# Kernel optimization log

Measured on AMD Instinct MI355X. Metric: run time of the kernel, lower is better.

The kernel has to match this reference:

```python
import jax, jax.numpy as jnp
import numpy as np

K = 8               # top-k frequencies
PRED_LEN = 96       # prediction_length
LOW_FREQ = 1        # low_frequency cutoff (drops DC)


def setup_inputs() -> dict:
    key = jax.random.key(0)
    x = jax.random.normal(key, (32, 2048, 64), dtype=jnp.float32)
    return {"x": x}


def reference(x):
    b, t, d = x.shape
    x_freq = jnp.fft.rfft(x, axis=1)                 # (b, t//2+1, d) complex
    freqs = jnp.fft.rfftfreq(t).astype(x.dtype)
    if t % 2 == 0:
        x_freq = x_freq[:, LOW_FREQ:-1]              # drop DC and Nyquist
        f = freqs[LOW_FREQ:-1]
    else:
        x_freq = x_freq[:, LOW_FREQ:]
        f = freqs[LOW_FREQ:]

    # top-k over frequency dim (axis=1), independently per (b, d)
    mag = jnp.abs(x_freq)                            # (b, F, d)
    _, idx = jax.lax.top_k(jnp.moveaxis(mag, 1, 2), K)  # (b, d, K), sorted desc
    idx = jnp.moveaxis(idx, 1, 2)                    # (b, K, d)
    x_k = jnp.take_along_axis(x_freq, idx, axis=1)   # (b, K, d) complex
    f_k = f[idx]                                     # (b, K, d)

    # extrapolate: add conjugate (negative) frequencies, then cos-sum
    x2 = jnp.concatenate([x_k, jnp.conj(x_k)], axis=1)  # (b, 2K, d)
    f2 = jnp.concatenate([f_k, -f_k], axis=1)           # (b, 2K, d)
    t_val = jnp.arange(t + PRED_LEN, dtype=x.dtype)     # (T,)
    amp = jnp.abs(x2) / t                               # (b, 2K, d)
    phase = jnp.angle(x2)                               # (b, 2K, d)
    # (b, 2K, T, d) broadcast intermediate, reduced over freq axis
    x_time = amp[:, :, None, :] * jnp.cos(
        2.0 * np.float32(np.pi) * f2[:, :, None, :] * t_val[None, None, :, None]
        + phase[:, :, None, :]
    )
    return x_time.sum(axis=1)                        # (b, t+PRED_LEN, d)
```

## Files before the change

kernel.cpp:

```cpp
#include <hip/hip_runtime.h>
#include <math.h>

#define BB 32
#define TT 2048
#define DD 64
#define PRED 96
#define TP (TT + PRED)
#define KTOP 8
#define MARGIN 8e-4f
#define PI_D 3.14159265358979323846

__device__ __forceinline__ int br6(int l) { return (int)(__brev((unsigned)l) >> 26); }
static constexpr int BR4[16] = {0,8,4,12,2,10,6,14,1,9,5,13,3,11,7,15};
static constexpr float C32T[16] = {
    1.0f, 0.98078528040323044913f, 0.92387953251128675613f, 0.83146961230254523708f,
    0.70710678118654752440f, 0.55557023301960222474f, 0.38268343236508977173f, 0.19509032201612826785f,
    0.0f, -0.19509032201612826785f, -0.38268343236508977173f, -0.55557023301960222474f,
    -0.70710678118654752440f, -0.83146961230254523708f, -0.92387953251128675613f, -0.98078528040323044913f};
static constexpr float S32T[16] = {
    0.0f, 0.19509032201612826785f, 0.38268343236508977173f, 0.55557023301960222474f,
    0.70710678118654752440f, 0.83146961230254523708f, 0.92387953251128675613f, 0.98078528040323044913f,
    1.0f, 0.98078528040323044913f, 0.92387953251128675613f, 0.83146961230254523708f,
    0.70710678118654752440f, 0.55557023301960222474f, 0.38268343236508977173f, 0.19509032201612826785f};

__device__ __forceinline__ float2 ctw(float2 a, int m) {
    const float rev = (float)m * (1.0f / 2048.0f);
    const float c = __builtin_amdgcn_cosf(rev);
    const float s = __builtin_amdgcn_sinf(rev);
    return make_float2(a.x * c + a.y * s, a.y * c - a.x * s);
}

#define SRE(pr,a) POOL[9216 + (pr) * 4224 + (a)]
#define SIM(pr,a) POOL[9216 + (pr) * 4224 + 2112 + (a)]

__global__ __launch_bounds__(256, 2) void fused_kernel(const float* __restrict__ x,
                                                       float* __restrict__ out) {
    __shared__ float POOL[17664];
    __shared__ int   coefK[4][KTOP];
    __shared__ float coefR[4][KTOP], coefI[4][KTOP];

    const int t    = threadIdx.x;
    const int wv   = t >> 6, p = t & 63;
    const int pair = wv >> 1, w = wv & 1;
    const int bid  = blockIdx.x;
    const int xcd  = bid & 7;
    const int idx  = bid >> 3;
    const int b    = (idx >> 3) * 4 + (xcd >> 1);
    const int grp4 = (xcd & 1) * 8 + (idx & 7);
    const int dp   = grp4 * 2 + pair;
    const int ch   = grp4 * 4 + wv;

    const float2* xv = (const float2*)x;
    const size_t xbase = (size_t)b * TT * (DD / 2) + dp;
    const int rl = 2 * br6(p) + w;

    float2 v[16];
    #pragma unroll
    for (int i = 0; i < 16; ++i)
        v[i] = xv[xbase + (size_t)(128 * BR4[i] + rl) * (DD / 2)];

    #pragma unroll
    for (int s = 1; s <= 4; ++s) {
        const int m = 1 << s, half = m >> 1, stepw = 32 >> s;
        #pragma unroll
        for (int g = 0; g < 16; g += m) {
            #pragma unroll
            for (int j = 0; j < half; ++j) {
                const float c = C32T[j * stepw], sn = S32T[j * stepw];
                const int i0 = g + j, i1 = i0 + half;
                const float tr = c * v[i1].x + sn * v[i1].y;
                const float ti = c * v[i1].y - sn * v[i1].x;
                v[i1] = make_float2(v[i0].x - tr, v[i0].y - ti);
                v[i0] = make_float2(v[i0].x + tr, v[i0].y + ti);
            }
        }
    }

    #pragma unroll
    for (int q = 1; q < 16; ++q) v[q] = ctw(v[q], (rl * q) & (TT - 1));

    #pragma unroll
    for (int s = 1; s <= 6; ++s) {
        const int half = 1 << (s - 1);
        const float rev = (float)(p & (half - 1)) / (float)(1 << s);
        const float wc  = __builtin_amdgcn_cosf(rev);
        const float wsn = __builtin_amdgcn_sinf(rev);
        const bool  hi  = (p & half) != 0;
        #pragma unroll
        for (int q = 0; q < 16; ++q) {
            float2 pv;
            pv.x = __shfl_xor(v[q].x, half, 64);
            pv.y = __shfl_xor(v[q].y, half, 64);
            const float2 bsv = hi ? v[q] : pv;
            const float2 asv = hi ? pv : v[q];
            const float tr = wc * bsv.x + wsn * bsv.y;
            const float ti = wc * bsv.y - wsn * bsv.x;
            v[q] = hi ? make_float2(asv.x - tr, asv.y - ti)
                      : make_float2(asv.x + tr, asv.y + ti);
        }
    }

    {
        const int exw = pair * 4608 + w * 2304 + p * 36;
        #pragma unroll
        for (int c = 0; c < 8; ++c)
            *(float4*)&POOL[exw + 4 * c] =
                make_float4(v[2*c].x, v[2*c].y, v[2*c+1].x, v[2*c+1].y);
    }
    __syncthreads();
    {
        const int exr = pair * 4608 + (1 - w) * 2304 + p * 36;
        const float revp = (float)p * (1.0f / 128.0f);
        const float wc7 = __builtin_amdgcn_cosf(revp);
        const float ws7 = __builtin_amdgcn_sinf(revp);
        const int kb = 1024 * w + 16 * p;
        #pragma unroll
        for (int c = 0; c < 8; ++c) {
            const float4 g = *(const float4*)&POOL[exr + 4 * c];
            #pragma unroll
            for (int e = 0; e < 2; ++e) {
                const int q = 2 * c + e;
                const float2 pv = e ? make_float2(g.z, g.w) : make_float2(g.x, g.y);
                const float2 bsv = w ? v[q] : pv;
                const float2 asv = w ? pv : v[q];
                const float tr = wc7 * bsv.x + ws7 * bsv.y;
                const float ti = wc7 * bsv.y - ws7 * bsv.x;
                const int k = kb + q, a = k + (k >> 5);
                SRE(pair, a) = w ? (asv.x - tr) : (asv.x + tr);
                SIM(pair, a) = w ? (asv.y - ti) : (asv.y + ti);
            }
        }
    }
    __syncthreads();

    unsigned A[16];
    #pragma unroll
    for (int q = 0; q < 16; ++q) {
        const int k = 16 * p + q;
        unsigned kk = 0u;
        if (k != 0) {
            const int a1 = k + (k >> 5);
            const int pk = TT - k, a2 = pk + (pk >> 5);
            const float zr = SRE(pair, a1), zi = SIM(pair, a1);
            const float yr = SRE(pair, a2), yi = SIM(pair, a2);
            float cr, ci;
            if (w == 0) { cr = 0.5f * (zr + yr); ci = 0.5f * (zi - yi); }
            else        { cr = 0.5f * (zi + yi); ci = 0.5f * (yr - zr); }
            const float mg = cr * cr + ci * ci;
            kk = (__float_as_uint(mg) & 0xFFFFF800u) | (unsigned)(2047 - k);
        }
        A[q] = kk;
    }

    #pragma unroll
    for (int sz = 2; sz <= 16; sz <<= 1) {
        #pragma unroll
        for (int d = sz >> 1; d > 0; d >>= 1) {
            #pragma unroll
            for (int i2 = 0; i2 < 16; ++i2) {
                const int j2i = i2 ^ d;
                if (j2i > i2) {
                    const bool desc = ((i2 & sz) == 0);
                    const unsigned a = A[i2], b2 = A[j2i];
                    const unsigned mx = a > b2 ? a : b2, mn = a > b2 ? b2 : a;
                    A[i2] = desc ? mx : mn;  A[j2i] = desc ? mn : mx;
                }
            }
        }
    }
    #pragma unroll
    for (int off = 1; off <= 32; off <<= 1) {
        unsigned Bv[16];
        #pragma unroll
        for (int i2 = 0; i2 < 16; ++i2)
            Bv[i2] = (unsigned)__shfl_xor((int)A[i2], off, 64);
        #pragma unroll
        for (int i2 = 0; i2 < 16; ++i2) {
            const unsigned o = Bv[15 - i2];
            A[i2] = A[i2] > o ? A[i2] : o;
        }
        #pragma unroll
        for (int d = 8; d > 0; d >>= 1) {
            #pragma unroll
            for (int i2 = 0; i2 < 16; ++i2) {
                if ((i2 & d) == 0) {
                    const int j2i = i2 + d;
                    const unsigned a = A[i2], b2 = A[j2i];
                    A[i2] = a > b2 ? a : b2;  A[j2i] = a > b2 ? b2 : a;
                }
            }
        }
    }

    const float m8f = __uint_as_float(A[7] & 0xFFFFF800u);
    unsigned bandmask = 0u;
    #pragma unroll
    for (int r = 0; r < 16; ++r) {
        const float mr = __uint_as_float(A[r] & 0xFFFFF800u);
        if (fabsf(mr - m8f) <= MARGIN * m8f) bandmask |= (1u << r);
    }
    const int flg = (bandmask != (1u << 7)) ? 1 : 0;

    unsigned myk = 0u;
    #pragma unroll
    for (int i2 = 0; i2 < 16; ++i2) myk = (p == i2) ? A[i2] : myk;
    const int kcand = 2047 - (int)(myk & 0x7FFu);

    if (!flg && p < KTOP) {
        const int k = kcand, a1 = k + (k >> 5), pk = TT - k, a2 = pk + (pk >> 5);
        const float zr = SRE(pair, a1), zi = SIM(pair, a1);
        const float yr = SRE(pair, a2), yi = SIM(pair, a2);
        float cr, ci;
        if (w == 0) { cr = 0.5f * (zr + yr); ci = 0.5f * (zi - yi); }
        else        { cr = 0.5f * (zi + yi); ci = 0.5f * (yr - zr); }
        coefK[wv][p] = k;
        coefR[wv][p] = cr * (2.0f / (float)TT);
        coefI[wv][p] = ci * (2.0f / (float)TT);
    }

    if (flg) {
        float sv[32];
        const float* xs = x + (size_t)b * TT * DD + ch;
        #pragma unroll
        for (int m2 = 0; m2 < 32; ++m2)
            sv[m2] = xs[(size_t)(p + 64 * m2) * DD];
        const double thA = -2.0 * PI_D * (double)p / 64.0;
        const double thB = -2.0 * PI_D * (double)p / (double)TT;
        const double wac = cos(thA), was = sin(thA);
        const double wbc = cos(thB), wbs = sin(thB);

        const unsigned bm = bandmask;
        const int lo = (int)__builtin_ctz(bm);
        double myM = 0.0, myR = 0.0, myI = 0.0;
        for (int r = 0; r < 16; ++r) {
            if (!((bm >> r) & 1u)) continue;
            const int kr = __shfl(kcand, r, 64);
            double ar = 0.0, ai = 0.0;
            for (int m2 = 0; m2 < 32; ++m2) {
                const int n  = p + 64 * m2;
                const int mm = (n * kr) & (TT - 1);
                const double qc  = __shfl(wac, mm >> 5, 64);
                const double qs  = __shfl(was, mm >> 5, 64);
                const double rc2 = __shfl(wbc, mm & 31, 64);
                const double rs2 = __shfl(wbs, mm & 31, 64);
                const double wr = qc * rc2 - qs * rs2;
                const double wi = qc * rs2 + qs * rc2;
                ar = fma((double)sv[m2], wr, ar);
                ai = fma((double)sv[m2], wi, ai);
            }
            #pragma unroll
            for (int off = 32; off; off >>= 1) {
                ar += __shfl_xor(ar, off, 64);
                ai += __shfl_xor(ai, off, 64);
            }
            if (p == r) { myM = ar * ar + ai * ai; myR = ar; myI = ai; }
        }
        const int h16 = p & 15;
        const double selfM = __shfl(myM, h16, 64);
        const int    selfK = __shfl(kcand, h16, 64);
        int rb = 0;
        for (int r2 = 0; r2 < 16; ++r2) {
            if (!((bm >> r2) & 1u)) continue;
            const double om = __shfl(myM, r2, 64);
            const int    ok = __shfl(kcand, r2, 64);
            if (r2 != h16 && (om > selfM || (om == selfM && ok < selfK))) ++rb;
        }
        const int isband = (int)((bm >> h16) & 1u);
        const int rank = isband ? (lo + rb) : h16;
        if (p < 16 && rank < KTOP) {
            coefK[wv][rank] = kcand;
            if (isband) {
                coefR[wv][rank] = (float)(myR * (2.0 / (double)TT));
                coefI[wv][rank] = (float)(myI * (2.0 / (double)TT));
            } else {
                const int k = kcand, a1 = k + (k >> 5), pk = TT - k, a2 = pk + (pk >> 5);
                const float zr = SRE(pair, a1), zi = SIM(pair, a1);
                const float yr = SRE(pair, a2), yi = SIM(pair, a2);
                float cr, ci;
                if (w == 0) { cr = 0.5f * (zr + yr); ci = 0.5f * (zi - yi); }
                else        { cr = 0.5f * (zi + yi); ci = 0.5f * (yr - zr); }
                coefR[wv][rank] = cr * (2.0f / (float)TT);
                coefI[wv][rank] = ci * (2.0f / (float)TT);
            }
        }
    }
    __syncthreads();

    const int d4 = t & 3, tq = t >> 2;
    int   kc[KTOP];
    float fr[KTOP], fi[KTOP], pc[KTOP], ps[KTOP], rc[KTOP], rs[KTOP];
    #pragma unroll
    for (int pp = 0; pp < KTOP; ++pp) {
        kc[pp] = coefK[d4][pp];
        fr[pp] = coefR[d4][pp];
        fi[pp] = coefI[d4][pp];
        const int j0 = (kc[pp] * tq) & (TT - 1);
        const float rv0 = (float)j0 * (1.0f / 2048.0f);
        pc[pp] = __builtin_amdgcn_cosf(rv0);
        ps[pp] = __builtin_amdgcn_sinf(rv0);
        const int jr = (kc[pp] * 64) & (TT - 1);
        const float rvr = (float)jr * (1.0f / 2048.0f);
        rc[pp] = __builtin_amdgcn_cosf(rvr);
        rs[pp] = __builtin_amdgcn_sinf(rvr);
    }
    float* ob = out + (size_t)b * TP * DD + grp4 * 4 + d4;
    #pragma unroll 2
    for (int m = 0; m < 34; ++m) {
        const int tv = tq + 64 * m;
        float acc = 0.0f;
        #pragma unroll
        for (int pp = 0; pp < KTOP; ++pp) acc += fr[pp] * pc[pp] - fi[pp] * ps[pp];
        if (tv < TP) ob[(size_t)tv * DD] = acc;
        #pragma unroll
        for (int pp = 0; pp < KTOP; ++pp) {
            const float nc = pc[pp] * rc[pp] - ps[pp] * rs[pp];
            const float ns = pc[pp] * rs[pp] + ps[pp] * rc[pp];
            pc[pp] = nc; ps[pp] = ns;
        }
    }
}

extern "C" void kernel_launch(void* const* d_in, const int* in_sizes, int n_in,
                              void* d_out, int out_size, void* d_ws, size_t ws_size,
                              hipStream_t stream) {
    const float* x = (const float*)d_in[0];
    float* out = (float*)d_out;
    (void)d_ws; (void)ws_size; (void)in_sizes; (void)n_in; (void)out_size;

    fused_kernel<<<BB * 16, 256, 0, stream>>>(x, out);
}
```

Before: 97.47 us.

## Split each channel pair's FFT across four waves to double the block count

Each block now handles one complex channel pair (two real channels) instead of two pairs. Each of the four waves holds 8 points instead of 16, and an extra cross-wave radix-2 stage is done through shared memory. Shared memory per block is roughly halved and launch bounds are raised to 4 blocks per CU, so the grid doubles to 1024 blocks for more occupancy and parallelism. In exchange there is an extra exchange round with its barriers, and only two of the four waves do the top-k selection, leaving the other waves idle during that phase.

```diff
diff --git a/kernel.cpp b/kernel.cpp
--- a/kernel.cpp
+++ b/kernel.cpp
@@ -11,7 +11,7 @@
 #define PI_D 3.14159265358979323846
 
 __device__ __forceinline__ int br6(int l) { return (int)(__brev((unsigned)l) >> 26); }
-static constexpr int BR4[16] = {0,8,4,12,2,10,6,14,1,9,5,13,3,11,7,15};
+static constexpr int BR3[8] = {0,4,2,6,1,5,3,7};
 static constexpr float C32T[16] = {
     1.0f, 0.98078528040323044913f, 0.92387953251128675613f, 0.83146961230254523708f,
     0.70710678118654752440f, 0.55557023301960222474f, 0.38268343236508977173f, 0.19509032201612826785f,
@@ -30,40 +30,39 @@
     return make_float2(a.x * c + a.y * s, a.y * c - a.x * s);
 }
 
-#define SRE(pr,a) POOL[9216 + (pr) * 4224 + (a)]
-#define SIM(pr,a) POOL[9216 + (pr) * 4224 + 2112 + (a)]
-
-__global__ __launch_bounds__(256, 2) void fused_kernel(const float* __restrict__ x,
+#define EXB(wvi,pi) ((wvi) * 1152 + (pi) * 18)
+#define SRE(a) POOL[4608 + (a)]
+#define SIM(a) POOL[6720 + (a)]
+
+__global__ __launch_bounds__(256, 4) void fused_kernel(const float* __restrict__ x,
                                                        float* __restrict__ out) {
-    __shared__ float POOL[17664];
-    __shared__ int   coefK[4][KTOP];
-    __shared__ float coefR[4][KTOP], coefI[4][KTOP];
+    __shared__ float POOL[8832];
+    __shared__ int   coefK[2][KTOP];
+    __shared__ float coefR[2][KTOP], coefI[2][KTOP];
 
     const int t    = threadIdx.x;
     const int wv   = t >> 6, p = t & 63;
-    const int pair = wv >> 1, w = wv & 1;
     const int bid  = blockIdx.x;
     const int xcd  = bid & 7;
     const int idx  = bid >> 3;
-    const int b    = (idx >> 3) * 4 + (xcd >> 1);
-    const int grp4 = (xcd & 1) * 8 + (idx & 7);
-    const int dp   = grp4 * 2 + pair;
-    const int ch   = grp4 * 4 + wv;
+    const int b    = ((idx >> 3) << 1) | (xcd >> 2);
+    const int dp   = ((xcd & 3) << 3) | (idx & 7);
 
     const float2* xv = (const float2*)x;
     const size_t xbase = (size_t)b * TT * (DD / 2) + dp;
-    const int rl = 2 * br6(p) + w;
-
-    float2 v[16];
-    #pragma unroll
-    for (int i = 0; i < 16; ++i)
-        v[i] = xv[xbase + (size_t)(128 * BR4[i] + rl) * (DD / 2)];
-
-    #pragma unroll
-    for (int s = 1; s <= 4; ++s) {
+    const int br2wv = ((wv & 1) << 1) | ((wv >> 1) & 1);
+    const int rl = 4 * br6(p) + br2wv;
+
+    float2 v[8];
+    #pragma unroll
+    for (int i = 0; i < 8; ++i)
+        v[i] = xv[xbase + (size_t)(256 * BR3[i] + rl) * (DD / 2)];
+
+    #pragma unroll
+    for (int s = 1; s <= 3; ++s) {
         const int m = 1 << s, half = m >> 1, stepw = 32 >> s;
         #pragma unroll
-        for (int g = 0; g < 16; g += m) {
+        for (int g = 0; g < 8; g += m) {
             #pragma unroll
             for (int j = 0; j < half; ++j) {
                 const float c = C32T[j * stepw], sn = S32T[j * stepw];
@@ -77,7 +76,7 @@
     }
 
     #pragma unroll
-    for (int q = 1; q < 16; ++q) v[q] = ctw(v[q], (rl * q) & (TT - 1));
+    for (int q = 1; q < 8; ++q) v[q] = ctw(v[q], (rl * q) & (TT - 1));
 
     #pragma unroll
     for (int s = 1; s <= 6; ++s) {
@@ -87,7 +86,7 @@
         const float wsn = __builtin_amdgcn_sinf(rev);
         const bool  hi  = (p & half) != 0;
         #pragma unroll
-        for (int q = 0; q < 16; ++q) {
+        for (int q = 0; q < 8; ++q) {
             float2 pv;
             pv.x = __shfl_xor(v[q].x, half, 64);
             pv.y = __shfl_xor(v[q].y, half, 64);
@@ -101,212 +100,236 @@
     }
 
     {
-        const int exw = pair * 4608 + w * 2304 + p * 36;
-        #pragma unroll
-        for (int c = 0; c < 8; ++c)
-            *(float4*)&POOL[exw + 4 * c] =
-                make_float4(v[2*c].x, v[2*c].y, v[2*c+1].x, v[2*c+1].y);
+        const int exw = EXB(wv, p);
+        #pragma unroll
+        for (int q = 0; q < 8; ++q) *(float2*)&POOL[exw + 2 * q] = v[q];
     }
     __syncthreads();
     {
-        const int exr = pair * 4608 + (1 - w) * 2304 + p * 36;
-        const float revp = (float)p * (1.0f / 128.0f);
-        const float wc7 = __builtin_amdgcn_cosf(revp);
-        const float ws7 = __builtin_amdgcn_sinf(revp);
-        const int kb = 1024 * w + 16 * p;
-        #pragma unroll
-        for (int c = 0; c < 8; ++c) {
-            const float4 g = *(const float4*)&POOL[exr + 4 * c];
-            #pragma unroll
-            for (int e = 0; e < 2; ++e) {
-                const int q = 2 * c + e;
-                const float2 pv = e ? make_float2(g.z, g.w) : make_float2(g.x, g.y);
-                const float2 bsv = w ? v[q] : pv;
-                const float2 asv = w ? pv : v[q];
-                const float tr = wc7 * bsv.x + ws7 * bsv.y;
-                const float ti = wc7 * bsv.y - ws7 * bsv.x;
-                const int k = kb + q, a = k + (k >> 5);
-                SRE(pair, a) = w ? (asv.x - tr) : (asv.x + tr);
-                SIM(pair, a) = w ? (asv.y - ti) : (asv.y + ti);
-            }
-        }
-    }
-    __syncthreads();
-
-    unsigned A[16];
-    #pragma unroll
-    for (int q = 0; q < 16; ++q) {
-        const int k = 16 * p + q;
-        unsigned kk = 0u;
-        if (k != 0) {
-            const int a1 = k + (k >> 5);
-            const int pk = TT - k, a2 = pk + (pk >> 5);
-            const float zr = SRE(pair, a1), zi = SIM(pair, a1);
-            const float yr = SRE(pair, a2), yi = SIM(pair, a2);
+        const int exr = EXB(wv ^ 1, p);
+        const float rev7 = (float)p * (1.0f / 128.0f);
+        const float c7 = __builtin_amdgcn_cosf(rev7);
+        const float s7 = __builtin_amdgcn_sinf(rev7);
+        const bool hi7 = (wv & 1) != 0;
+        #pragma unroll
+        for (int q = 0; q < 8; ++q) {
+            const float2 pv = *(const float2*)&POOL[exr + 2 * q];
+            const float2 bsv = hi7 ? v[q] : pv;
+            const float2 asv = hi7 ? pv : v[q];
+            const float tr = c7 * bsv.x + s7 * bsv.y;
+            const float ti = c7 * bsv.y - s7 * bsv.x;
+            v[q] = hi7 ? make_float2(asv.x - tr, asv.y - ti)
+                       : make_float2(asv.x + tr, asv.y + ti);
+        }
+    }
+    __syncthreads();
+
+    {
+        const int exw = EXB(wv, p);
+        #pragma unroll
+        for (int q = 0; q < 8; ++q) *(float2*)&POOL[exw + 2 * q] = v[q];
+    }
+    __syncthreads();
+    {
+        const int exr = EXB(wv ^ 2, p);
+        const float rev8 = (float)(64 * (wv & 1) + p) * (1.0f / 256.0f);
+        const float c8 = __builtin_amdgcn_cosf(rev8);
+        const float s8 = __builtin_amdgcn_sinf(rev8);
+        const bool hi8 = ((wv >> 1) & 1) != 0;
+        const int kb = 512 * wv + 8 * p;
+        #pragma unroll
+        for (int q = 0; q < 8; ++q) {
+            const float2 pv = *(const float2*)&POOL[exr + 2 * q];
+            const float2 bsv = hi8 ? v[q] : pv;
+            const float2 asv = hi8 ? pv : v[q];
+            const float tr = c8 * bsv.x + s8 * bsv.y;
+            const float ti = c8 * bsv.y - s8 * bsv.x;
+            const float re = hi8 ? (asv.x - tr) : (asv.x + tr);
+            const float im = hi8 ? (asv.y - ti) : (asv.y + ti);
+            const int k = kb + q, a = k + (k >> 5);
+            SRE(a) = re;
+            SIM(a) = im;
+        }
+    }
+    __syncthreads();
+
+    if (wv < 2) {
+        const int w = wv;
+        unsigned A[16];
+        #pragma unroll
+        for (int q = 0; q < 16; ++q) {
+            const int k = 16 * p + q;
+            unsigned kk = 0u;
+            if (k != 0) {
+                const int a1 = k + (k >> 5);
+                const int pk = TT - k, a2 = pk + (pk >> 5);
+                const float zr = SRE(a1), zi = SIM(a1);
+                const float yr = SRE(a2), yi = SIM(a2);
+                float cr, ci;
+                if (w == 0) { cr = 0.5f * (zr + yr); ci = 0.5f * (zi - yi); }
+                else        { cr = 0.5f * (zi + yi); ci = 0.5f * (yr - zr); }
+                const float mg = cr * cr + ci * ci;
+                kk = (__float_as_uint(mg) & 0xFFFFF800u) | (unsigned)(2047 - k);
+            }
+            A[q] = kk;
+        }
+
+        #pragma unroll
+        for (int sz = 2; sz <= 16; sz <<= 1) {
+            #pragma unroll
+            for (int d = sz >> 1; d > 0; d >>= 1) {
+                #pragma unroll
+                for (int i2 = 0; i2 < 16; ++i2) {
+                    const int j2i = i2 ^ d;
+                    if (j2i > i2) {
+                        const bool desc = ((i2 & sz) == 0);
+                        const unsigned a = A[i2], b2 = A[j2i];
+                        const unsigned mx = a > b2 ? a : b2, mn = a > b2 ? b2 : a;
+                        A[i2] = desc ? mx : mn;  A[j2i] = desc ? mn : mx;
+                    }
+                }
+            }
+        }
+        #pragma unroll
+        for (int off = 1; off <= 32; off <<= 1) {
+            unsigned Bv[16];
+            #pragma unroll
+            for (int i2 = 0; i2 < 16; ++i2)
+                Bv[i2] = (unsigned)__shfl_xor((int)A[i2], off, 64);
+            #pragma unroll
+            for (int i2 = 0; i2 < 16; ++i2) {
+                const unsigned o = Bv[15 - i2];
+                A[i2] = A[i2] > o ? A[i2] : o;
+            }
+            #pragma unroll
+            for (int d = 8; d > 0; d >>= 1) {
+                #pragma unroll
+                for (int i2 = 0; i2 < 16; ++i2) {
+                    if ((i2 & d) == 0) {
+                        const int j2i = i2 + d;
+                        const unsigned a = A[i2], b2 = A[j2i];
+                        A[i2] = a > b2 ? a : b2;  A[j2i] = a > b2 ? b2 : a;
+                    }
+                }
+            }
+        }
+
+        const float m8f = __uint_as_float(A[7] & 0xFFFFF800u);
+        unsigned bandmask = 0u;
+        #pragma unroll
+        for (int r = 0; r < 16; ++r) {
+            const float mr = __uint_as_float(A[r] & 0xFFFFF800u);
+            if (fabsf(mr - m8f) <= MARGIN * m8f) bandmask |= (1u << r);
+        }
+        const int flg = (bandmask != (1u << 7)) ? 1 : 0;
+
+        unsigned myk = 0u;
+        #pragma unroll
+        for (int i2 = 0; i2 < 16; ++i2) myk = (p == i2) ? A[i2] : myk;
+        const int kcand = 2047 - (int)(myk & 0x7FFu);
+
+        if (!flg && p < KTOP) {
+            const int k = kcand, a1 = k + (k >> 5), pk = TT - k, a2 = pk + (pk >> 5);
+            const float zr = SRE(a1), zi = SIM(a1);
+            const float yr = SRE(a2), yi = SIM(a2);
             float cr, ci;
             if (w == 0) { cr = 0.5f * (zr + yr); ci = 0.5f * (zi - yi); }
             else        { cr = 0.5f * (zi + yi); ci = 0.5f * (yr - zr); }
-            const float mg = cr * cr + ci * ci;
-            kk = (__float_as_uint(mg) & 0xFFFFF800u) | (unsigned)(2047 - k);
-        }
-        A[q] = kk;
-    }
-
-    #pragma unroll
-    for (int sz = 2; sz <= 16; sz <<= 1) {
-        #pragma unroll
-        for (int d = sz >> 1; d > 0; d >>= 1) {
-            #pragma unroll
-            for (int i2 = 0; i2 < 16; ++i2) {
-                const int j2i = i2 ^ d;
-                if (j2i > i2) {
-                    const bool desc = ((i2 & sz) == 0);
-                    const unsigned a = A[i2], b2 = A[j2i];
-                    const unsigned mx = a > b2 ? a : b2, mn = a > b2 ? b2 : a;
-                    A[i2] = desc ? mx : mn;  A[j2i] = desc ? mn : mx;
-                }
-            }
-        }
-    }
-    #pragma unroll
-    for (int off = 1; off <= 32; off <<= 1) {
-        unsigned Bv[16];
-        #pragma unroll
-        for (int i2 = 0; i2 < 16; ++i2)
-            Bv[i2] = (unsigned)__shfl_xor((int)A[i2], off, 64);
-        #pragma unroll
-        for (int i2 = 0; i2 < 16; ++i2) {
-            const unsigned o = Bv[15 - i2];
-            A[i2] = A[i2] > o ? A[i2] : o;
-        }
-        #pragma unroll
-        for (int d = 8; d > 0; d >>= 1) {
-            #pragma unroll
-            for (int i2 = 0; i2 < 16; ++i2) {
-                if ((i2 & d) == 0) {
-                    const int j2i = i2 + d;
-                    const unsigned a = A[i2], b2 = A[j2i];
-                    A[i2] = a > b2 ? a : b2;  A[j2i] = a > b2 ? b2 : a;
-                }
-            }
-        }
-    }
-
-    const float m8f = __uint_as_float(A[7] & 0xFFFFF800u);
-    unsigned bandmask = 0u;
-    #pragma unroll
-    for (int r = 0; r < 16; ++r) {
-        const float mr = __uint_as_float(A[r] & 0xFFFFF800u);
-        if (fabsf(mr - m8f) <= MARGIN * m8f) bandmask |= (1u << r);
-    }
-    const int flg = (bandmask != (1u << 7)) ? 1 : 0;
-
-    unsigned myk = 0u;
-    #pragma unroll
-    for (int i2 = 0; i2 < 16; ++i2) myk = (p == i2) ? A[i2] : myk;
-    const int kcand = 2047 - (int)(myk & 0x7FFu);
-
-    if (!flg && p < KTOP) {
-        const int k = kcand, a1 = k + (k >> 5), pk = TT - k, a2 = pk + (pk >> 5);
-        const float zr = SRE(pair, a1), zi = SIM(pair, a1);
-        const float yr = SRE(pair, a2), yi = SIM(pair, a2);
-        float cr, ci;
-        if (w == 0) { cr = 0.5f * (zr + yr); ci = 0.5f * (zi - yi); }
-        else        { cr = 0.5f * (zi + yi); ci = 0.5f * (yr - zr); }
-        coefK[wv][p] = k;
-        coefR[wv][p] = cr * (2.0f / (float)TT);
-        coefI[wv][p] = ci * (2.0f / (float)TT);
-    }
-
-    if (flg) {
-        float sv[32];
-        const float* xs = x + (size_t)b * TT * DD + ch;
-        #pragma unroll
-        for (int m2 = 0; m2 < 32; ++m2)
-            sv[m2] = xs[(size_t)(p + 64 * m2) * DD];
-        const double thA = -2.0 * PI_D * (double)p / 64.0;
-        const double thB = -2.0 * PI_D * (double)p / (double)TT;
-        const double wac = cos(thA), was = sin(thA);
-        const double wbc = cos(thB), wbs = sin(thB);
-
-        const unsigned bm = bandmask;
-        const int lo = (int)__builtin_ctz(bm);
-        double myM = 0.0, myR = 0.0, myI = 0.0;
-        for (int r = 0; r < 16; ++r) {
-            if (!((bm >> r) & 1u)) continue;
-            const int kr = __shfl(kcand, r, 64);
-            double ar = 0.0, ai = 0.0;
-            for (int m2 = 0; m2 < 32; ++m2) {
-                const int n  = p + 64 * m2;
-                const int mm = (n * kr) & (TT - 1);
-                const double qc  = __shfl(wac, mm >> 5, 64);
-                const double qs  = __shfl(was, mm >> 5, 64);
-                const double rc2 = __shfl(wbc, mm & 31, 64);
-                const double rs2 = __shfl(wbs, mm & 31, 64);
-                const double wr = qc * rc2 - qs * rs2;
-                const double wi = qc * rs2 + qs * rc2;
-                ar = fma((double)sv[m2], wr, ar);
-                ai = fma((double)sv[m2], wi, ai);
-            }
-            #pragma unroll
-            for (int off = 32; off; off >>= 1) {
-                ar += __shfl_xor(ar, off, 64);
-                ai += __shfl_xor(ai, off, 64);
-            }
-            if (p == r) { myM = ar * ar + ai * ai; myR = ar; myI = ai; }
-        }
-        const int h16 = p & 15;
-        const double selfM = __shfl(myM, h16, 64);
-        const int    selfK = __shfl(kcand, h16, 64);
-        int rb = 0;
-        for (int r2 = 0; r2 < 16; ++r2) {
-            if (!((bm >> r2) & 1u)) continue;
-            const double om = __shfl(myM, r2, 64);
-            const int    ok = __shfl(kcand, r2, 64);
-            if (r2 != h16 && (om > selfM || (om == selfM && ok < selfK))) ++rb;
-        }
-        const int isband = (int)((bm >> h16) & 1u);
-        const int rank = isband ? (lo + rb) : h16;
-        if (p < 16 && rank < KTOP) {
-            coefK[wv][rank] = kcand;
-            if (isband) {
-                coefR[wv][rank] = (float)(myR * (2.0 / (double)TT));
-                coefI[wv][rank] = (float)(myI * (2.0 / (double)TT));
-            } else {
-                const int k = kcand, a1 = k + (k >> 5), pk = TT - k, a2 = pk + (pk >> 5);
-                const float zr = SRE(pair, a1), zi = SIM(pair, a1);
-                const float yr = SRE(pair, a2), yi = SIM(pair, a2);
-                float cr, ci;
-                if (w == 0) { cr = 0.5f * (zr + yr); ci = 0.5f * (zi - yi); }
-                else        { cr = 0.5f * (zi + yi); ci = 0.5f * (yr - zr); }
-                coefR[wv][rank] = cr * (2.0f / (float)TT);
-                coefI[wv][rank] = ci * (2.0f / (float)TT);
-            }
-        }
-    }
-    __syncthreads();
-
-    const int d4 = t & 3, tq = t >> 2;
+            coefK[w][p] = k;
+            coefR[w][p] = cr * (2.0f / (float)TT);
+            coefI[w][p] = ci * (2.0f / (float)TT);
+        }
+
+        if (flg) {
+            float sv[32];
+            const float* xs = x + (size_t)b * TT * DD + 2 * dp + w;
+            #pragma unroll
+            for (int m2 = 0; m2 < 32; ++m2)
+                sv[m2] = xs[(size_t)(p + 64 * m2) * DD];
+            const double thA = -2.0 * PI_D * (double)p / 64.0;
+            const double thB = -2.0 * PI_D * (double)p / (double)TT;
+            const double wac = cos(thA), was = sin(thA);
+            const double wbc = cos(thB), wbs = sin(thB);
+
+            const unsigned bm = bandmask;
+            const int lo = (int)__builtin_ctz(bm);
+            double myM = 0.0, myR = 0.0, myI = 0.0;
+            for (int r = 0; r < 16; ++r) {
+                if (!((bm >> r) & 1u)) continue;
+                const int kr = __shfl(kcand, r, 64);
+                double ar = 0.0, ai = 0.0;
+                for (int m2 = 0; m2 < 32; ++m2) {
+                    const int n  = p + 64 * m2;
+                    const int mm = (n * kr) & (TT - 1);
+                    const double qc  = __shfl(wac, mm >> 5, 64);
+                    const double qs  = __shfl(was, mm >> 5, 64);
+                    const double rc2 = __shfl(wbc, mm & 31, 64);
+                    const double rs2 = __shfl(wbs, mm & 31, 64);
+                    const double wr = qc * rc2 - qs * rs2;
+                    const double wi = qc * rs2 + qs * rc2;
+                    ar = fma((double)sv[m2], wr, ar);
+                    ai = fma((double)sv[m2], wi, ai);
+                }
+                #pragma unroll
+                for (int off = 32; off; off >>= 1) {
+                    ar += __shfl_xor(ar, off, 64);
+                    ai += __shfl_xor(ai, off, 64);
+                }
+                if (p == r) { myM = ar * ar + ai * ai; myR = ar; myI = ai; }
+            }
+            const int h16 = p & 15;
+            const double selfM = __shfl(myM, h16, 64);
+            const int    selfK = __shfl(kcand, h16, 64);
+            int rb = 0;
+            for (int r2 = 0; r2 < 16; ++r2) {
+                if (!((bm >> r2) & 1u)) continue;
+                const double om = __shfl(myM, r2, 64);
+                const int    ok = __shfl(kcand, r2, 64);
+                if (r2 != h16 && (om > selfM || (om == selfM && ok < selfK))) ++rb;
+            }
+            const int isband = (int)((bm >> h16) & 1u);
+            const int rank = isband ? (lo + rb) : h16;
+            if (p < 16 && rank < KTOP) {
+                coefK[w][rank] = kcand;
+                if (isband) {
+                    coefR[w][rank] = (float)(myR * (2.0 / (double)TT));
+                    coefI[w][rank] = (float)(myI * (2.0 / (double)TT));
+                } else {
+                    const int k = kcand, a1 = k + (k >> 5), pk = TT - k, a2 = pk + (pk >> 5);
+                    const float zr = SRE(a1), zi = SIM(a1);
+                    const float yr = SRE(a2), yi = SIM(a2);
+                    float cr, ci;
+                    if (w == 0) { cr = 0.5f * (zr + yr); ci = 0.5f * (zi - yi); }
+                    else        { cr = 0.5f * (zi + yi); ci = 0.5f * (yr - zr); }
+                    coefR[w][rank] = cr * (2.0f / (float)TT);
+                    coefI[w][rank] = ci * (2.0f / (float)TT);
+                }
+            }
+        }
+    }
+    __syncthreads();
+
+    const int d2 = t & 1, tq = t >> 1;
     int   kc[KTOP];
     float fr[KTOP], fi[KTOP], pc[KTOP], ps[KTOP], rc[KTOP], rs[KTOP];
     #pragma unroll
     for (int pp = 0; pp < KTOP; ++pp) {
-        kc[pp] = coefK[d4][pp];
-        fr[pp] = coefR[d4][pp];
-        fi[pp] = coefI[d4][pp];
+        kc[pp] = coefK[d2][pp];
+        fr[pp] = coefR[d2][pp];
+        fi[pp] = coefI[d2][pp];
         const int j0 = (kc[pp] * tq) & (TT - 1);
         const float rv0 = (float)j0 * (1.0f / 2048.0f);
         pc[pp] = __builtin_amdgcn_cosf(rv0);
         ps[pp] = __builtin_amdgcn_sinf(rv0);
-        const int jr = (kc[pp] * 64) & (TT - 1);
+        const int jr = (kc[pp] * 128) & (TT - 1);
         const float rvr = (float)jr * (1.0f / 2048.0f);
         rc[pp] = __builtin_amdgcn_cosf(rvr);
         rs[pp] = __builtin_amdgcn_sinf(rvr);
     }
-    float* ob = out + (size_t)b * TP * DD + grp4 * 4 + d4;
+    float* ob = out + (size_t)b * TP * DD + 2 * dp + d2;
     #pragma unroll 2
-    for (int m = 0; m < 34; ++m) {
-        const int tv = tq + 64 * m;
+    for (int m = 0; m < 17; ++m) {
+        const int tv = tq + 128 * m;
         float acc = 0.0f;
         #pragma unroll
         for (int pp = 0; pp < KTOP; ++pp) acc += fr[pp] * pc[pp] - fi[pp] * ps[pp];
@@ -327,5 +350,5 @@
     float* out = (float*)d_out;
     (void)d_ws; (void)ws_size; (void)in_sizes; (void)n_in; (void)out_size;
 
-    fused_kernel<<<BB * 16, 256, 0, stream>>>(x, out);
+    fused_kernel<<<BB * 32, 256, 0, stream>>>(x, out);
 }
```

Measured after the change: 98.85 us. Within noise of the previous version (+1.4%).
